# Performance work log

Hardware: AMD Instinct MI355X
Metric: run time of the kernel (lower is better)

## Reference

```python
import jax, jax.numpy as jnp
import numpy as np

N = 64          # Hilbert space dim
B = 4096        # batch of density matrices
K = 2           # number of jump operators
DT = 0.01       # time step
C = (0.0, 0.5, 1.0)
A = ((0.0, 0.0, 0.0), (0.5, 0.0, 0.0), (0.0, 1.0, 0.0))
BW = (1.0 / 6.0, 2.0 / 3.0, 1.0 / 6.0)
NEUMANN_ORDER = 2


def _dag(M):
    # real-valued reference: dagger == transpose on last two axes
    return jnp.swapaxes(M, -1, -2)


def _sandwich(M, rho):
    # M rho M^dag ; M:[N,N], rho:[B,N,N]
    return M @ rho @ _dag(M)


def _dissipator(L, rho):
    # sum_k L_k rho L_k^dag ; L:[K,N,N], rho:[B,N,N]
    return jnp.einsum('kij,bjl,kml->bim', L, rho, L)


def _neumann_ratio(Ui, Uj, I):
    # U(ci) U(cj)^{-1} with U(cj)^{-1} ~ sum_{p<=order} (I - U(cj))^p
    W = I - Uj
    inv = I
    Wp = I
    for _ in range(NEUMANN_ORDER):
        Wp = Wp @ W
        inv = inv + Wp
    return Ui @ inv


def _forward(rho0, U_half, U_one, L0, Lh, L1):
    I = jnp.eye(N, dtype=rho0.dtype)
    Umap = {0.0: I, 0.5: U_half, 1.0: U_one}
    Lmap = {0.0: L0, 0.5: Lh, 1.0: L1}

    def ratio(ci, cj):
        if ci == cj:
            return I
        if cj == 0.0:
            return Umap[ci]
        return _neumann_ratio(Umap[ci], Umap[cj], I)

    # intermediate stages rho^(i)
    stages = []
    for i, ci in enumerate(C):
        rho_i = rho0 if ci == 0.0 else _sandwich(Umap[ci], rho0)
        for j in range(i):
            a_ij = A[i][j]
            if a_ij == 0.0:
                continue
            cj = C[j]
            P_ij = ratio(ci, cj)
            rho_i = rho_i + DT * a_ij * _sandwich(P_ij, _dissipator(Lmap[cj], stages[j]))
        stages.append(rho_i)

    # output combination
    rho_new = _sandwich(Umap[1.0], rho0)
    for i, bi in enumerate(BW):
        if bi == 0.0:
            continue
        ci = C[i]
        Q_i = ratio(1.0, ci)
        rho_new = rho_new + DT * bi * _sandwich(Q_i, _dissipator(Lmap[ci], stages[i]))
    return rho_new


def setup_inputs() -> dict:
    key = jax.random.key(0)
    k1, k2, k3, k4, k5, k6 = jax.random.split(key, 6)
    I = jnp.eye(N, dtype=jnp.float32)
    rho0 = jax.random.normal(k1, (B, N, N), dtype=jnp.float32)
    rho0 = 0.5 * (rho0 + jnp.swapaxes(rho0, -1, -2))  # hermitian-like
    # no-jump propagators: near-identity so the Neumann series is sane
    U_half = I + 0.02 * jax.random.normal(k2, (N, N), dtype=jnp.float32)
    U_one = I + 0.04 * jax.random.normal(k3, (N, N), dtype=jnp.float32)
    L0 = 0.1 * jax.random.normal(k4, (K, N, N), dtype=jnp.float32)
    Lh = 0.1 * jax.random.normal(k5, (K, N, N), dtype=jnp.float32)
    L1 = 0.1 * jax.random.normal(k6, (K, N, N), dtype=jnp.float32)
    return {"rho0": rho0, "U_half": U_half, "U_one": U_one,
            "L0": L0, "Lh": Lh, "L1": L1}


def reference(rho0, U_half, U_one, L0, Lh, L1):
    return _forward(rho0, U_half, U_one, L0, Lh, L1)
```

## Files before the change

### kernel.cpp

```cpp
#include <hip/hip_runtime.h>
#include <hip/hip_bf16.h>

#define NDIM 64
#define BP   72
#define DT_  0.01f

typedef __attribute__((ext_vector_type(8)))  short bf16x8;
typedef __attribute__((ext_vector_type(16))) float f32x16;

struct Frag { bf16x8 f[4]; };


__device__ __forceinline__ unsigned short f2b(float x) {
    __hip_bfloat16 h = __float2bfloat16(x);
    return __builtin_bit_cast(unsigned short, h);
}
__device__ __forceinline__ float b2f(unsigned short u) {
    unsigned int v = (unsigned int)u << 16;
    return __builtin_bit_cast(float, v);
}
__device__ __forceinline__ unsigned int f2b2(float lo, float hi) {
    return (unsigned int)f2b(lo) | ((unsigned int)f2b(hi) << 16);
}


__device__ __forceinline__ bf16x8 ldfrag(const unsigned short* M, int rb, int j, int ln, int hq) {
    return *(const bf16x8*)&M[(rb + ln) * BP + j * 16 + hq * 8];
}

__device__ __forceinline__ void ldg_op(Frag& F, const unsigned short* __restrict__ p,
                                       int ln, int hq, int cw) {
#pragma unroll
    for (int j = 0; j < 4; ++j)
        F.f[j] = *(const bf16x8*)&p[(cw + ln) * 64 + j * 16 + hq * 8];
}

__device__ __forceinline__ void ldWfrag(Frag& F, const float* __restrict__ Uh,
                                        int ln, int hq, int cw) {
    const int n = cw + ln;
#pragma unroll
    for (int j = 0; j < 4; ++j) {
        const int k0 = j * 16 + hq * 8;
        const float* q = &Uh[n * 64 + k0];
        float4 u = *(const float4*)q;
        float4 v = *(const float4*)(q + 4);
        float wv[8] = {-u.x, -u.y, -u.z, -u.w, -v.x, -v.y, -v.z, -v.w};
#pragma unroll
        for (int e = 0; e < 8; ++e)
            if (n == k0 + e) wv[e] += 1.f;
        uint4 o;
        o.x = f2b2(wv[0], wv[1]); o.y = f2b2(wv[2], wv[3]);
        o.z = f2b2(wv[4], wv[5]); o.w = f2b2(wv[6], wv[7]);
        F.f[j] = __builtin_bit_cast(bf16x8, o);
    }
}

template <bool ACC>
__device__ __forceinline__ void ntg(const unsigned short* A, const Frag& F, f32x16& acc,
                                    int ln, int hq, int rb) {
    if (!ACC) {
#pragma unroll
        for (int r = 0; r < 16; ++r) acc[r] = 0.f;
    }
#pragma unroll
    for (int j = 0; j < 4; ++j)
        acc = __builtin_amdgcn_mfma_f32_32x32x16_bf16(ldfrag(A, rb, j, ln, hq), F.f[j], acc, 0, 0, 0);
}

__device__ __forceinline__ void ntg2(const unsigned short* A, const Frag& Fa, const Frag& Fb,
                                     f32x16& c0, f32x16& c1, int ln, int hq, int rb) {
#pragma unroll
    for (int r = 0; r < 16; ++r) { c0[r] = 0.f; c1[r] = 0.f; }
#pragma unroll
    for (int j = 0; j < 4; ++j) {
        bf16x8 a = ldfrag(A, rb, j, ln, hq);
        c0 = __builtin_amdgcn_mfma_f32_32x32x16_bf16(a, Fa.f[j], c0, 0, 0, 0);
        c1 = __builtin_amdgcn_mfma_f32_32x32x16_bf16(a, Fb.f[j], c1, 0, 0, 0);
    }
}

__device__ __forceinline__ void stT(unsigned short* D, const f32x16& v,
                                    int ln, int hq, int rw, int cw) {
#pragma unroll
    for (int g = 0; g < 4; ++g) {
        uint2 o;
        o.x = f2b2(v[4 * g + 0], v[4 * g + 1]);
        o.y = f2b2(v[4 * g + 2], v[4 * g + 3]);
        *(uint2*)&D[(cw + ln) * BP + rw + 8 * g + 4 * hq] = o;
    }
}

__device__ __forceinline__ void ldT(float* r, const unsigned short* S,
                                    int ln, int hq, int rw, int cw) {
#pragma unroll
    for (int g = 0; g < 4; ++g) {
        uint2 u = *(const uint2*)&S[(cw + ln) * BP + rw + 8 * g + 4 * hq];
        unsigned short o[4];
        *(uint2*)o = u;
#pragma unroll
        for (int j = 0; j < 4; ++j) r[4 * g + j] = b2f(o[j]);
    }
}


__global__ void __launch_bounds__(256) krk_setup(const float* __restrict__ Uh,
                                                 const float* __restrict__ U1,
                                                 const float* __restrict__ L0,
                                                 const float* __restrict__ Lh,
                                                 const float* __restrict__ L1,
                                                 unsigned short* __restrict__ ws) {
    __shared__ unsigned short sW [NDIM * BP];
    __shared__ unsigned short sWt[NDIM * BP];

    const int blk = blockIdx.x, tid = threadIdx.x;

    if (blk < 8) {
        const float* srcs[8] = {Uh, U1, L0, L0 + 4096, Lh, Lh + 4096, L1, L1 + 4096};
        const float* s = srcs[blk];
        unsigned short* d = ws + blk * 4096;
#pragma unroll
        for (int i = 0; i < 4; ++i) {
            int flat = (tid + i * 256) * 4;
            float4 v = *(const float4*)&s[flat];
            uint2 o; o.x = f2b2(v.x, v.y); o.y = f2b2(v.z, v.w);
            *(uint2*)&d[flat] = o;
        }
        return;
    }

    const int lane = tid & 63, w = tid >> 6, ln = lane & 31, hq = lane >> 5;
    const int rw = 32 * (w >> 1), cw = 32 * (w & 1);

#pragma unroll
    for (int i = 0; i < 4; ++i) {
        int flat = (tid + i * 256) * 4;
        int r = flat >> 6, c = flat & 63;
        float4 u = *(const float4*)&Uh[flat];
        float wv[4] = {-u.x, -u.y, -u.z, -u.w};
#pragma unroll
        for (int j = 0; j < 4; ++j)
            if (r == c + j) wv[j] += 1.f;
        unsigned short o[4] = {f2b(wv[0]), f2b(wv[1]), f2b(wv[2]), f2b(wv[3])};
        *(uint2*)&sW[r * BP + c] = *(uint2*)o;
#pragma unroll
        for (int j = 0; j < 4; ++j) sWt[(c + j) * BP + r] = o[j];
    }
    Frag Fw;
    ldWfrag(Fw, Uh, ln, hq, cw);
    __syncthreads();

    f32x16 t0;
    ntg<false>(sWt, Fw, t0, ln, hq, rw);
    float wts[16];
    ldT(wts, sW, ln, hq, rw, cw);
    unsigned short* ws8 = ws + 8 * 4096;
#pragma unroll
    for (int g = 0; g < 4; ++g) {
        uint2 o;
        float v0, v1;
#pragma unroll
        for (int j = 0; j < 4; j += 2) {
            int r0 = 4 * g + j, r1 = r0 + 1;
            int row0 = rw + (r0 & 3) + 8 * g + 4 * hq;
            int row1 = row0 + 1;
            v0 = ((row0 == cw + ln) ? 1.f : 0.f) + wts[r0] + t0[r0];
            v1 = ((row1 == cw + ln) ? 1.f : 0.f) + wts[r1] + t0[r1];
            if (j == 0) o.x = f2b2(v0, v1); else o.y = f2b2(v0, v1);
        }
        *(uint2*)&ws8[(cw + ln) * 64 + rw + 8 * g + 4 * hq] = o;
    }
}


__global__ void __launch_bounds__(256, 2) krk_main(const float* __restrict__ rho0,
                                                   const unsigned short* __restrict__ ws,
                                                   float* __restrict__ out) {
    __shared__ unsigned short Bb[2][4][NDIM * BP];

    const int tid = threadIdx.x;
    const int w = tid >> 6, lane = tid & 63, ln = lane & 31, hq = lane >> 5;
    const int rw = 32 * (w >> 1), cw = 32 * (w & 1);

    const float c12 = 0.5f * DT_, c16 = DT_ / 6.f, c23 = 2.f * DT_ / 3.f;

    f32x16 t0[2], t1[2], s0[2], a1[2];
    Frag Fa, Fb, Fc;

#pragma unroll
    for (int m = 0; m < 2; ++m) {
        const float* rho = rho0 + (size_t)(2 * blockIdx.x + m) * (NDIM * NDIM);
#pragma unroll
        for (int i = 0; i < 4; ++i) {
            int flat = (tid + i * 256) * 4;
            int r = flat >> 6, c = flat & 63;
            float4 v = *(const float4*)&rho[flat];
            uint2 o; o.x = f2b2(v.x, v.y); o.y = f2b2(v.z, v.w);
            *(uint2*)&Bb[m][0][r * BP + c] = o;
        }
    }
    ldg_op(Fa, ws + 2 * 4096, ln, hq, cw);
    ldg_op(Fb, ws + 3 * 4096, ln, hq, cw);
    __syncthreads();

#pragma unroll
    for (int m = 0; m < 2; ++m)
        ntg2(Bb[m][0], Fa, Fb, t0[m], t1[m], ln, hq, rw);
#pragma unroll
    for (int m = 0; m < 2; ++m) {
        stT(Bb[m][1], t0[m], ln, hq, rw, cw);
        stT(Bb[m][2], t1[m], ln, hq, rw, cw);
    }
    __syncthreads();

#pragma unroll
    for (int m = 0; m < 2; ++m) {
        ntg<false>(Bb[m][1], Fa, s0[m], ln, hq, rw);
        ntg<true >(Bb[m][2], Fb, s0[m], ln, hq, rw);
    }
#pragma unroll
    for (int m = 0; m < 2; ++m) {
        float r0s[16];
        ldT(r0s, Bb[m][0], ln, hq, rw, cw);
        f32x16 X;
#pragma unroll
        for (int r = 0; r < 16; ++r) X[r] = r0s[r] + c12 * s0[m][r];
        stT(Bb[m][0], X, ln, hq, rw, cw);
    }
    ldg_op(Fc, ws + 0 * 4096, ln, hq, cw);
    __syncthreads();

#pragma unroll
    for (int m = 0; m < 2; ++m)
        ntg<false>(Bb[m][0], Fc, t0[m], ln, hq, rw);
#pragma unroll
    for (int m = 0; m < 2; ++m)
        stT(Bb[m][3], t0[m], ln, hq, rw, cw);
    __syncthreads();

#pragma unroll
    for (int m = 0; m < 2; ++m)
        ntg<false>(Bb[m][3], Fc, t0[m], ln, hq, rw);
#pragma unroll
    for (int m = 0; m < 2; ++m)
        stT(Bb[m][1], t0[m], ln, hq, rw, cw);
    ldg_op(Fa, ws + 4 * 4096, ln, hq, cw);
    ldg_op(Fb, ws + 5 * 4096, ln, hq, cw);
    __syncthreads();

#pragma unroll
    for (int m = 0; m < 2; ++m)
        ntg2(Bb[m][1], Fa, Fb, t0[m], t1[m], ln, hq, rw);
#pragma unroll
    for (int m = 0; m < 2; ++m) {
        stT(Bb[m][2], t0[m], ln, hq, rw, cw);
        stT(Bb[m][3], t1[m], ln, hq, rw, cw);
    }
    __syncthreads();

#pragma unroll
    for (int m = 0; m < 2; ++m) {
        ntg<false>(Bb[m][2], Fa, t0[m], ln, hq, rw);
        ntg<true >(Bb[m][3], Fb, t0[m], ln, hq, rw);
    }
#pragma unroll
    for (int m = 0; m < 2; ++m)
        stT(Bb[m][1], t0[m], ln, hq, rw, cw);
    ldg_op(Fc, ws + 8 * 4096, ln, hq, cw);
    __syncthreads();

#pragma unroll
    for (int m = 0; m < 2; ++m)
        ntg<false>(Bb[m][1], Fc, t0[m], ln, hq, rw);
#pragma unroll
    for (int m = 0; m < 2; ++m)
        stT(Bb[m][2], t0[m], ln, hq, rw, cw);
    __syncthreads();

#pragma unroll
    for (int m = 0; m < 2; ++m) {
        f32x16 h1;
        ntg<false>(Bb[m][2], Fc, h1, ln, hq, rw);
        float xs[16];
        ldT(xs, Bb[m][0], ln, hq, rw, cw);
#pragma unroll
        for (int r = 0; r < 16; ++r) {
            t0[m][r] = xs[r] + (c16 - c12) * s0[m][r] + c23 * h1[r];
            t1[m][r] = xs[r] - c12 * s0[m][r] + DT_ * h1[r];
        }
        stT(Bb[m][1], t0[m], ln, hq, rw, cw);
        stT(Bb[m][3], t1[m], ln, hq, rw, cw);
    }
    ldg_op(Fc, ws + 1 * 4096, ln, hq, cw);
    __syncthreads();

#pragma unroll
    for (int m = 0; m < 2; ++m) {
        ntg<false>(Bb[m][1], Fc, t0[m], ln, hq, rw);
        ntg<false>(Bb[m][3], Fc, t1[m], ln, hq, rw);
    }
#pragma unroll
    for (int m = 0; m < 2; ++m) {
        stT(Bb[m][0], t0[m], ln, hq, rw, cw);
        stT(Bb[m][2], t1[m], ln, hq, rw, cw);
    }
    __syncthreads();

#pragma unroll
    for (int m = 0; m < 2; ++m) {
        ntg<false>(Bb[m][0], Fc, a1[m], ln, hq, rw);
        ntg<false>(Bb[m][2], Fc, t0[m], ln, hq, rw);
    }
#pragma unroll
    for (int m = 0; m < 2; ++m)
        stT(Bb[m][1], t0[m], ln, hq, rw, cw);
    ldg_op(Fa, ws + 6 * 4096, ln, hq, cw);
    ldg_op(Fb, ws + 7 * 4096, ln, hq, cw);
    __syncthreads();

#pragma unroll
    for (int m = 0; m < 2; ++m)
        ntg2(Bb[m][1], Fa, Fb, t0[m], t1[m], ln, hq, rw);
#pragma unroll
    for (int m = 0; m < 2; ++m) {
        stT(Bb[m][0], t0[m], ln, hq, rw, cw);
        stT(Bb[m][2], t1[m], ln, hq, rw, cw);
    }
    __syncthreads();

#pragma unroll
    for (int m = 0; m < 2; ++m) {
        ntg<false>(Bb[m][0], Fa, t0[m], ln, hq, rw);
        ntg<true >(Bb[m][2], Fb, t0[m], ln, hq, rw);
        float* o = out + (size_t)(2 * blockIdx.x + m) * (NDIM * NDIM);
#pragma unroll
        for (int g = 0; g < 4; ++g) {
            float4 v;
            v.x = a1[m][4 * g + 0] + c16 * t0[m][4 * g + 0];
            v.y = a1[m][4 * g + 1] + c16 * t0[m][4 * g + 1];
            v.z = a1[m][4 * g + 2] + c16 * t0[m][4 * g + 2];
            v.w = a1[m][4 * g + 3] + c16 * t0[m][4 * g + 3];
            *(float4*)&o[(cw + ln) * 64 + rw + 8 * g + 4 * hq] = v;
        }
    }
}


extern "C" void kernel_launch(void* const* d_in, const int* in_sizes, int n_in,
                              void* d_out, int out_size, void* d_ws, size_t ws_size,
                              hipStream_t stream) {
    const float* rho0 = (const float*)d_in[0];
    const float* Uh   = (const float*)d_in[1];
    const float* U1   = (const float*)d_in[2];
    const float* L0   = (const float*)d_in[3];
    const float* Lh   = (const float*)d_in[4];
    const float* L1   = (const float*)d_in[5];
    float* out = (float*)d_out;
    unsigned short* ws = (unsigned short*)d_ws;

    int Bn = in_sizes[0] / (NDIM * NDIM);

    krk_setup<<<9, 256, 0, stream>>>(Uh, U1, L0, Lh, L1, ws);
    krk_main<<<Bn / 2, 256, 0, stream>>>(rho0, ws, out);
}
```

Measured before the change: 159.1 us.

## Swizzle LDS tiles, cut buffers to three per matrix, raise occupancy

```diff
diff --git a/kernel.cpp b/kernel.cpp
--- a/kernel.cpp
+++ b/kernel.cpp
@@ -2,8 +2,9 @@
 #include <hip/hip_bf16.h>
 
 #define NDIM 64
-#define BP   72
 #define DT_  0.01f
+
+#define SWZ(row, boff) ((((row)) << 7) + ((boff) ^ (((row) & 7) << 4)))
 
 typedef __attribute__((ext_vector_type(8)))  short bf16x8;
 typedef __attribute__((ext_vector_type(16))) float f32x16;
@@ -25,7 +26,8 @@
 
 
 __device__ __forceinline__ bf16x8 ldfrag(const unsigned short* M, int rb, int j, int ln, int hq) {
-    return *(const bf16x8*)&M[(rb + ln) * BP + j * 16 + hq * 8];
+    const int row = rb + ln;
+    return *(const bf16x8*)((const char*)M + SWZ(row, 32 * j + 16 * hq));
 }
 
 __device__ __forceinline__ void ldg_op(Frag& F, const unsigned short* __restrict__ p,
@@ -81,25 +83,40 @@
 
 __device__ __forceinline__ void stT(unsigned short* D, const f32x16& v,
                                     int ln, int hq, int rw, int cw) {
+    const int row = cw + ln;
 #pragma unroll
     for (int g = 0; g < 4; ++g) {
         uint2 o;
         o.x = f2b2(v[4 * g + 0], v[4 * g + 1]);
         o.y = f2b2(v[4 * g + 2], v[4 * g + 3]);
-        *(uint2*)&D[(cw + ln) * BP + rw + 8 * g + 4 * hq] = o;
+        *(uint2*)((char*)D + SWZ(row, 2 * rw + 16 * g + 8 * hq)) = o;
     }
 }
 
 __device__ __forceinline__ void ldT(float* r, const unsigned short* S,
                                     int ln, int hq, int rw, int cw) {
+    const int row = cw + ln;
 #pragma unroll
     for (int g = 0; g < 4; ++g) {
-        uint2 u = *(const uint2*)&S[(cw + ln) * BP + rw + 8 * g + 4 * hq];
+        uint2 u = *(const uint2*)((const char*)S + SWZ(row, 2 * rw + 16 * g + 8 * hq));
         unsigned short o[4];
         *(uint2*)o = u;
 #pragma unroll
         for (int j = 0; j < 4; ++j) r[4 * g + j] = b2f(o[j]);
     }
+}
+
+__device__ __forceinline__ void ldTraw(uint2* r, const unsigned short* S,
+                                       int ln, int hq, int rw, int cw) {
+    const int row = cw + ln;
+#pragma unroll
+    for (int g = 0; g < 4; ++g)
+        r[g] = *(const uint2*)((const char*)S + SWZ(row, 2 * rw + 16 * g + 8 * hq));
+}
+__device__ __forceinline__ float rsf(const uint2* rs, int r) {
+    unsigned int wv = (r & 2) ? rs[r >> 2].y : rs[r >> 2].x;
+    unsigned short u = (r & 1) ? (unsigned short)(wv >> 16) : (unsigned short)(wv & 0xffffu);
+    return b2f(u);
 }
 
 
@@ -109,8 +126,8 @@
                                                  const float* __restrict__ Lh,
                                                  const float* __restrict__ L1,
                                                  unsigned short* __restrict__ ws) {
-    __shared__ unsigned short sW [NDIM * BP];
-    __shared__ unsigned short sWt[NDIM * BP];
+    __shared__ unsigned short sW [NDIM * NDIM];
+    __shared__ unsigned short sWt[NDIM * NDIM];
 
     const int blk = blockIdx.x, tid = threadIdx.x;
 
@@ -141,9 +158,10 @@
         for (int j = 0; j < 4; ++j)
             if (r == c + j) wv[j] += 1.f;
         unsigned short o[4] = {f2b(wv[0]), f2b(wv[1]), f2b(wv[2]), f2b(wv[3])};
-        *(uint2*)&sW[r * BP + c] = *(uint2*)o;
-#pragma unroll
-        for (int j = 0; j < 4; ++j) sWt[(c + j) * BP + r] = o[j];
+        *(uint2*)((char*)sW + SWZ(r, 2 * c)) = *(uint2*)o;
+#pragma unroll
+        for (int j = 0; j < 4; ++j)
+            *(unsigned short*)((char*)sWt + SWZ(c + j, 2 * r)) = o[j];
     }
     Frag Fw;
     ldWfrag(Fw, Uh, ln, hq, cw);
@@ -172,10 +190,10 @@
 }
 
 
-__global__ void __launch_bounds__(256, 2) krk_main(const float* __restrict__ rho0,
+__global__ void __launch_bounds__(256, 3) krk_main(const float* __restrict__ rho0,
                                                    const unsigned short* __restrict__ ws,
                                                    float* __restrict__ out) {
-    __shared__ unsigned short Bb[2][4][NDIM * BP];
+    __shared__ unsigned short Bb[2][3][NDIM * NDIM];
 
     const int tid = threadIdx.x;
     const int w = tid >> 6, lane = tid & 63, ln = lane & 31, hq = lane >> 5;
@@ -184,6 +202,7 @@
     const float c12 = 0.5f * DT_, c16 = DT_ / 6.f, c23 = 2.f * DT_ / 3.f;
 
     f32x16 t0[2], t1[2], s0[2], a1[2];
+    uint2 rs[2][4];
     Frag Fa, Fb, Fc;
 
 #pragma unroll
@@ -195,7 +214,7 @@
             int r = flat >> 6, c = flat & 63;
             float4 v = *(const float4*)&rho[flat];
             uint2 o; o.x = f2b2(v.x, v.y); o.y = f2b2(v.z, v.w);
-            *(uint2*)&Bb[m][0][r * BP + c] = o;
+            *(uint2*)((char*)Bb[m][0] + SWZ(r, 2 * c)) = o;
         }
     }
     ldg_op(Fa, ws + 2 * 4096, ln, hq, cw);
@@ -206,6 +225,9 @@
     for (int m = 0; m < 2; ++m)
         ntg2(Bb[m][0], Fa, Fb, t0[m], t1[m], ln, hq, rw);
 #pragma unroll
+    for (int m = 0; m < 2; ++m)
+        ldTraw(rs[m], Bb[m][0], ln, hq, rw, cw);
+#pragma unroll
     for (int m = 0; m < 2; ++m) {
         stT(Bb[m][1], t0[m], ln, hq, rw, cw);
         stT(Bb[m][2], t1[m], ln, hq, rw, cw);
@@ -219,11 +241,9 @@
     }
 #pragma unroll
     for (int m = 0; m < 2; ++m) {
-        float r0s[16];
-        ldT(r0s, Bb[m][0], ln, hq, rw, cw);
         f32x16 X;
 #pragma unroll
-        for (int r = 0; r < 16; ++r) X[r] = r0s[r] + c12 * s0[m][r];
+        for (int r = 0; r < 16; ++r) X[r] = rsf(rs[m], r) + c12 * s0[m][r];
         stT(Bb[m][0], X, ln, hq, rw, cw);
     }
     ldg_op(Fc, ws + 0 * 4096, ln, hq, cw);
@@ -234,103 +254,107 @@
         ntg<false>(Bb[m][0], Fc, t0[m], ln, hq, rw);
 #pragma unroll
     for (int m = 0; m < 2; ++m)
-        stT(Bb[m][3], t0[m], ln, hq, rw, cw);
-    __syncthreads();
-
-#pragma unroll
-    for (int m = 0; m < 2; ++m)
-        ntg<false>(Bb[m][3], Fc, t0[m], ln, hq, rw);
-#pragma unroll
-    for (int m = 0; m < 2; ++m)
         stT(Bb[m][1], t0[m], ln, hq, rw, cw);
+    __syncthreads();
+
+#pragma unroll
+    for (int m = 0; m < 2; ++m)
+        ntg<false>(Bb[m][1], Fc, t0[m], ln, hq, rw);
+#pragma unroll
+    for (int m = 0; m < 2; ++m)
+        stT(Bb[m][2], t0[m], ln, hq, rw, cw);
     ldg_op(Fa, ws + 4 * 4096, ln, hq, cw);
     ldg_op(Fb, ws + 5 * 4096, ln, hq, cw);
     __syncthreads();
 
 #pragma unroll
     for (int m = 0; m < 2; ++m)
-        ntg2(Bb[m][1], Fa, Fb, t0[m], t1[m], ln, hq, rw);
-#pragma unroll
-    for (int m = 0; m < 2; ++m) {
+        ntg2(Bb[m][2], Fa, Fb, t0[m], t1[m], ln, hq, rw);
+#pragma unroll
+    for (int m = 0; m < 2; ++m) {
+        stT(Bb[m][0], t0[m], ln, hq, rw, cw);
+        stT(Bb[m][1], t1[m], ln, hq, rw, cw);
+    }
+    __syncthreads();
+
+#pragma unroll
+    for (int m = 0; m < 2; ++m) {
+        ntg<false>(Bb[m][0], Fa, t0[m], ln, hq, rw);
+        ntg<true >(Bb[m][1], Fb, t0[m], ln, hq, rw);
+    }
+#pragma unroll
+    for (int m = 0; m < 2; ++m)
         stT(Bb[m][2], t0[m], ln, hq, rw, cw);
-        stT(Bb[m][3], t1[m], ln, hq, rw, cw);
-    }
-    __syncthreads();
-
-#pragma unroll
-    for (int m = 0; m < 2; ++m) {
-        ntg<false>(Bb[m][2], Fa, t0[m], ln, hq, rw);
-        ntg<true >(Bb[m][3], Fb, t0[m], ln, hq, rw);
-    }
-#pragma unroll
-    for (int m = 0; m < 2; ++m)
-        stT(Bb[m][1], t0[m], ln, hq, rw, cw);
     ldg_op(Fc, ws + 8 * 4096, ln, hq, cw);
     __syncthreads();
 
 #pragma unroll
     for (int m = 0; m < 2; ++m)
+        ntg<false>(Bb[m][2], Fc, t0[m], ln, hq, rw);
+#pragma unroll
+    for (int m = 0; m < 2; ++m)
+        stT(Bb[m][0], t0[m], ln, hq, rw, cw);
+    __syncthreads();
+
+#pragma unroll
+    for (int m = 0; m < 2; ++m) {
+        f32x16 h1;
+        ntg<false>(Bb[m][0], Fc, h1, ln, hq, rw);
+        f32x16 M1, M2;
+#pragma unroll
+        for (int r = 0; r < 16; ++r) {
+            float rv = rsf(rs[m], r);
+            M1[r] = rv + c16 * s0[m][r] + c23 * h1[r];
+            M2[r] = rv + DT_ * h1[r];
+        }
+        stT(Bb[m][1], M1, ln, hq, rw, cw);
+        stT(Bb[m][2], M2, ln, hq, rw, cw);
+    }
+    ldg_op(Fc, ws + 1 * 4096, ln, hq, cw);
+    __syncthreads();
+
+#pragma unroll
+    for (int m = 0; m < 2; ++m)
         ntg<false>(Bb[m][1], Fc, t0[m], ln, hq, rw);
 #pragma unroll
     for (int m = 0; m < 2; ++m)
+        stT(Bb[m][0], t0[m], ln, hq, rw, cw);
+    __syncthreads();
+
+#pragma unroll
+    for (int m = 0; m < 2; ++m) {
+        ntg<false>(Bb[m][0], Fc, a1[m], ln, hq, rw);
+        ntg<false>(Bb[m][2], Fc, t1[m], ln, hq, rw);
+    }
+#pragma unroll
+    for (int m = 0; m < 2; ++m)
+        stT(Bb[m][1], t1[m], ln, hq, rw, cw);
+    __syncthreads();
+
+#pragma unroll
+    for (int m = 0; m < 2; ++m)
+        ntg<false>(Bb[m][1], Fc, t0[m], ln, hq, rw);
+#pragma unroll
+    for (int m = 0; m < 2; ++m)
         stT(Bb[m][2], t0[m], ln, hq, rw, cw);
-    __syncthreads();
-
-#pragma unroll
-    for (int m = 0; m < 2; ++m) {
-        f32x16 h1;
-        ntg<false>(Bb[m][2], Fc, h1, ln, hq, rw);
-        float xs[16];
-        ldT(xs, Bb[m][0], ln, hq, rw, cw);
-#pragma unroll
-        for (int r = 0; r < 16; ++r) {
-            t0[m][r] = xs[r] + (c16 - c12) * s0[m][r] + c23 * h1[r];
-            t1[m][r] = xs[r] - c12 * s0[m][r] + DT_ * h1[r];
-        }
-        stT(Bb[m][1], t0[m], ln, hq, rw, cw);
-        stT(Bb[m][3], t1[m], ln, hq, rw, cw);
-    }
-    ldg_op(Fc, ws + 1 * 4096, ln, hq, cw);
-    __syncthreads();
-
-#pragma unroll
-    for (int m = 0; m < 2; ++m) {
-        ntg<false>(Bb[m][1], Fc, t0[m], ln, hq, rw);
-        ntg<false>(Bb[m][3], Fc, t1[m], ln, hq, rw);
-    }
-#pragma unroll
-    for (int m = 0; m < 2; ++m) {
-        stT(Bb[m][0], t0[m], ln, hq, rw, cw);
-        stT(Bb[m][2], t1[m], ln, hq, rw, cw);
-    }
-    __syncthreads();
-
-#pragma unroll
-    for (int m = 0; m < 2; ++m) {
-        ntg<false>(Bb[m][0], Fc, a1[m], ln, hq, rw);
-        ntg<false>(Bb[m][2], Fc, t0[m], ln, hq, rw);
-    }
-#pragma unroll
-    for (int m = 0; m < 2; ++m)
-        stT(Bb[m][1], t0[m], ln, hq, rw, cw);
     ldg_op(Fa, ws + 6 * 4096, ln, hq, cw);
     ldg_op(Fb, ws + 7 * 4096, ln, hq, cw);
     __syncthreads();
 
 #pragma unroll
     for (int m = 0; m < 2; ++m)
-        ntg2(Bb[m][1], Fa, Fb, t0[m], t1[m], ln, hq, rw);
+        ntg2(Bb[m][2], Fa, Fb, t0[m], t1[m], ln, hq, rw);
 #pragma unroll
     for (int m = 0; m < 2; ++m) {
         stT(Bb[m][0], t0[m], ln, hq, rw, cw);
-        stT(Bb[m][2], t1[m], ln, hq, rw, cw);
+        stT(Bb[m][1], t1[m], ln, hq, rw, cw);
     }
     __syncthreads();
 
 #pragma unroll
     for (int m = 0; m < 2; ++m) {
         ntg<false>(Bb[m][0], Fa, t0[m], ln, hq, rw);
-        ntg<true >(Bb[m][2], Fb, t0[m], ln, hq, rw);
+        ntg<true >(Bb[m][1], Fb, t0[m], ln, hq, rw);
         float* o = out + (size_t)(2 * blockIdx.x + m) * (NDIM * NDIM);
 #pragma unroll
         for (int g = 0; g < 4; ++g) {
```

Measured after the change: 177.2 us. +11.4%, slower.

## Collapse RK stages into sum of precomputed sandwich operators per batch

Applied to the files above, without the earlier changes.

```diff
diff --git a/kernel.cpp b/kernel.cpp
--- a/kernel.cpp
+++ b/kernel.cpp
@@ -4,6 +4,7 @@
 #define NDIM 64
 #define BP   72
 #define DT_  0.01f
+#define NTERM 23
 
 typedef __attribute__((ext_vector_type(8)))  short bf16x8;
 typedef __attribute__((ext_vector_type(16))) float f32x16;
@@ -33,6 +34,27 @@
 #pragma unroll
     for (int j = 0; j < 4; ++j)
         F.f[j] = *(const bf16x8*)&p[(cw + ln) * 64 + j * 16 + hq * 8];
+}
+
+__device__ __forceinline__ void ldsF(Frag& F, const unsigned short* p, int ln, int hq, int cw) {
+#pragma unroll
+    for (int j = 0; j < 4; ++j)
+        F.f[j] = *(const bf16x8*)&p[(cw + ln) * BP + j * 16 + hq * 8];
+}
+
+__device__ __forceinline__ void ldg_opF32(Frag& F, const float* __restrict__ P,
+                                          int ln, int hq, int cw) {
+    const int n = cw + ln;
+#pragma unroll
+    for (int j = 0; j < 4; ++j) {
+        const float* q = &P[n * 64 + j * 16 + hq * 8];
+        float4 u = *(const float4*)q;
+        float4 v = *(const float4*)(q + 4);
+        uint4 o;
+        o.x = f2b2(u.x, u.y); o.y = f2b2(u.z, u.w);
+        o.z = f2b2(v.x, v.y); o.w = f2b2(v.z, v.w);
+        F.f[j] = __builtin_bit_cast(bf16x8, o);
+    }
 }
 
 __device__ __forceinline__ void ldWfrag(Frag& F, const float* __restrict__ Uh,
@@ -67,16 +89,12 @@
         acc = __builtin_amdgcn_mfma_f32_32x32x16_bf16(ldfrag(A, rb, j, ln, hq), F.f[j], acc, 0, 0, 0);
 }
 
-__device__ __forceinline__ void ntg2(const unsigned short* A, const Frag& Fa, const Frag& Fb,
-                                     f32x16& c0, f32x16& c1, int ln, int hq, int rb) {
-#pragma unroll
-    for (int r = 0; r < 16; ++r) { c0[r] = 0.f; c1[r] = 0.f; }
-#pragma unroll
-    for (int j = 0; j < 4; ++j) {
-        bf16x8 a = ldfrag(A, rb, j, ln, hq);
-        c0 = __builtin_amdgcn_mfma_f32_32x32x16_bf16(a, Fa.f[j], c0, 0, 0, 0);
-        c1 = __builtin_amdgcn_mfma_f32_32x32x16_bf16(a, Fb.f[j], c1, 0, 0, 0);
-    }
+__device__ __forceinline__ f32x16 ntg_reg(const Frag& A, const Frag& F, const f32x16& Z) {
+    f32x16 a = __builtin_amdgcn_mfma_f32_32x32x16_bf16(A.f[0], F.f[0], Z, 0, 0, 0);
+#pragma unroll
+    for (int j = 1; j < 4; ++j)
+        a = __builtin_amdgcn_mfma_f32_32x32x16_bf16(A.f[j], F.f[j], a, 0, 0, 0);
+    return a;
 }
 
 __device__ __forceinline__ void stT(unsigned short* D, const f32x16& v,
@@ -90,6 +108,15 @@
     }
 }
 
+__device__ __forceinline__ void stN(unsigned short* D, const f32x16& v,
+                                    int ln, int hq, int rw, int cw) {
+#pragma unroll
+    for (int r = 0; r < 16; ++r) {
+        int row = rw + (r & 3) + 8 * (r >> 2) + 4 * hq;
+        D[row * BP + (cw + ln)] = f2b(v[r]);
+    }
+}
+
 __device__ __forceinline__ void ldT(float* r, const unsigned short* S,
                                     int ln, int hq, int rw, int cw) {
 #pragma unroll
@@ -99,6 +126,17 @@
         *(uint2*)o = u;
 #pragma unroll
         for (int j = 0; j < 4; ++j) r[4 * g + j] = b2f(o[j]);
+    }
+}
+
+__device__ __forceinline__ void emit(unsigned short* __restrict__ g, const f32x16& v, float s,
+                                     int ln, int hq, int rw, int cw) {
+#pragma unroll
+    for (int gq = 0; gq < 4; ++gq) {
+        uint2 o;
+        o.x = f2b2(s * v[4 * gq + 0], s * v[4 * gq + 1]);
+        o.y = f2b2(s * v[4 * gq + 2], s * v[4 * gq + 3]);
+        *(uint2*)&g[(cw + ln) * 64 + rw + 8 * gq + 4 * hq] = o;
     }
 }
 
@@ -109,236 +147,207 @@
                                                  const float* __restrict__ Lh,
                                                  const float* __restrict__ L1,
                                                  unsigned short* __restrict__ ws) {
-    __shared__ unsigned short sW [NDIM * BP];
-    __shared__ unsigned short sWt[NDIM * BP];
-
-    const int blk = blockIdx.x, tid = threadIdx.x;
-
-    if (blk < 8) {
-        const float* srcs[8] = {Uh, U1, L0, L0 + 4096, Lh, Lh + 4096, L1, L1 + 4096};
-        const float* s = srcs[blk];
-        unsigned short* d = ws + blk * 4096;
-#pragma unroll
-        for (int i = 0; i < 4; ++i) {
-            int flat = (tid + i * 256) * 4;
-            float4 v = *(const float4*)&s[flat];
-            uint2 o; o.x = f2b2(v.x, v.y); o.y = f2b2(v.z, v.w);
-            *(uint2*)&d[flat] = o;
-        }
-        return;
-    }
-
+    __shared__ unsigned short B[7][NDIM * BP];
+
+    const int tid = threadIdx.x;
     const int lane = tid & 63, w = tid >> 6, ln = lane & 31, hq = lane >> 5;
     const int rw = 32 * (w >> 1), cw = 32 * (w & 1);
+
+    const float c12 = 0.5f * DT_, c16 = DT_ / 6.f, c23 = 2.f * DT_ / 3.f;
+    const float sA = sqrtf(c16);
+    const float sB = sqrtf(c23);
+    const float sC = sqrtf(c23 * c12);
+    const float sD = sqrtf(c16 * DT_);
+    const float sE = sqrtf(c16 * DT_ * c12);
 
 #pragma unroll
     for (int i = 0; i < 4; ++i) {
         int flat = (tid + i * 256) * 4;
         int r = flat >> 6, c = flat & 63;
         float4 u = *(const float4*)&Uh[flat];
-        float wv[4] = {-u.x, -u.y, -u.z, -u.w};
-#pragma unroll
-        for (int j = 0; j < 4; ++j)
-            if (r == c + j) wv[j] += 1.f;
-        unsigned short o[4] = {f2b(wv[0]), f2b(wv[1]), f2b(wv[2]), f2b(wv[3])};
-        *(uint2*)&sW[r * BP + c] = *(uint2*)o;
-#pragma unroll
-        for (int j = 0; j < 4; ++j) sWt[(c + j) * BP + r] = o[j];
-    }
-    Frag Fw;
+        const float* uf = (const float*)&u;
+        float wv[4];
+#pragma unroll
+        for (int j = 0; j < 4; ++j) wv[j] = ((r == c + j) ? 1.f : 0.f) - uf[j];
+#pragma unroll
+        for (int j = 0; j < 4; ++j) B[0][(c + j) * BP + r] = f2b(uf[j]);
+        uint2 ow; ow.x = f2b2(wv[0], wv[1]); ow.y = f2b2(wv[2], wv[3]);
+        *(uint2*)&B[4][r * BP + c] = ow;
+#pragma unroll
+        for (int j = 0; j < 4; ++j) B[5][(c + j) * BP + r] = f2b(wv[j]);
+
+        float4 p = *(const float4*)&U1[flat];
+        const float* pf = (const float*)&p;
+#pragma unroll
+        for (int j = 0; j < 4; ++j) B[1][(c + j) * BP + r] = f2b(pf[j]);
+        uint2 oq; oq.x = f2b2(p.x, p.y); oq.y = f2b2(p.z, p.w);
+        *(uint2*)&ws[flat] = oq;
+
+        float4 a = *(const float4*)&L0[flat];
+        const float* af = (const float*)&a;
+#pragma unroll
+        for (int j = 0; j < 4; ++j) B[2][(c + j) * BP + r] = f2b(af[j]);
+        float4 b = *(const float4*)&L0[4096 + flat];
+        const float* bf = (const float*)&b;
+#pragma unroll
+        for (int j = 0; j < 4; ++j) B[3][(c + j) * BP + r] = f2b(bf[j]);
+    }
+
+    Frag FUh, FU1, FLh0, FLh1, F10, F11, Fw;
+    ldg_opF32(FUh,  Uh,        ln, hq, cw);
+    ldg_opF32(FU1,  U1,        ln, hq, cw);
+    ldg_opF32(FLh0, Lh,        ln, hq, cw);
+    ldg_opF32(FLh1, Lh + 4096, ln, hq, cw);
+    ldg_opF32(F10,  L1,        ln, hq, cw);
+    ldg_opF32(F11,  L1 + 4096, ln, hq, cw);
     ldWfrag(Fw, Uh, ln, hq, cw);
     __syncthreads();
 
-    f32x16 t0;
-    ntg<false>(sWt, Fw, t0, ln, hq, rw);
-    float wts[16];
-    ldT(wts, sW, ln, hq, rw, cw);
-    unsigned short* ws8 = ws + 8 * 4096;
-#pragma unroll
-    for (int g = 0; g < 4; ++g) {
-        uint2 o;
-        float v0, v1;
-#pragma unroll
-        for (int j = 0; j < 4; j += 2) {
-            int r0 = 4 * g + j, r1 = r0 + 1;
-            int row0 = rw + (r0 & 3) + 8 * g + 4 * hq;
-            int row1 = row0 + 1;
-            v0 = ((row0 == cw + ln) ? 1.f : 0.f) + wts[r0] + t0[r0];
-            v1 = ((row1 == cw + ln) ? 1.f : 0.f) + wts[r1] + t0[r1];
-            if (j == 0) o.x = f2b2(v0, v1); else o.y = f2b2(v0, v1);
-        }
-        *(uint2*)&ws8[(cw + ln) * 64 + rw + 8 * g + 4 * hq] = o;
-    }
-}
-
-
-__global__ void __launch_bounds__(256, 2) krk_main(const float* __restrict__ rho0,
+    f32x16 e;
+
+    {
+        f32x16 t0;
+        ntg<false>(B[5], Fw, t0, ln, hq, rw);
+        float wts[16];
+        ldT(wts, B[4], ln, hq, rw, cw);
+#pragma unroll
+        for (int g = 0; g < 4; ++g) {
+            float vv[4];
+#pragma unroll
+            for (int i = 0; i < 4; ++i) {
+                int r = 4 * g + i;
+                int row = rw + i + 8 * g + 4 * hq;
+                vv[i] = ((row == cw + ln) ? 1.f : 0.f) + wts[r] + t0[r];
+            }
+            uint2 o; o.x = f2b2(vv[0], vv[1]); o.y = f2b2(vv[2], vv[3]);
+            *(uint2*)&B[6][(cw + ln) * BP + rw + 8 * g + 4 * hq] = o;
+        }
+    }
+    ntg<false>(B[2], FU1, e, ln, hq, rw); emit(ws + 1 * 4096, e, sA, ln, hq, rw, cw);
+    ntg<false>(B[3], FU1, e, ln, hq, rw); emit(ws + 2 * 4096, e, sA, ln, hq, rw, cw);
+    ntg<false>(B[1], F10, e, ln, hq, rw); emit(ws + 9 * 4096, e, sA, ln, hq, rw, cw);
+    ntg<false>(B[1], F11, e, ln, hq, rw); emit(ws + 10 * 4096, e, sA, ln, hq, rw, cw);
+    __syncthreads();
+
+    Frag FV; ldsF(FV, B[6], ln, hq, cw);
+
+    ntg<false>(B[2], FUh, e, ln, hq, rw); stN(B[4], e, ln, hq, rw, cw);
+    ntg<false>(B[3], FUh, e, ln, hq, rw); stN(B[5], e, ln, hq, rw, cw);
+    __syncthreads();
+
+    ntg<false>(B[0], FLh0, e, ln, hq, rw); stN(B[1], e, ln, hq, rw, cw);
+    ntg<false>(B[0], FLh1, e, ln, hq, rw); stN(B[2], e, ln, hq, rw, cw);
+    __syncthreads();
+
+    ntg<false>(B[1], FV, e, ln, hq, rw); stN(B[3], e, ln, hq, rw, cw);
+    ntg<false>(B[2], FV, e, ln, hq, rw); stN(B[0], e, ln, hq, rw, cw);
+    __syncthreads();
+
+    ntg<false>(B[3], FU1, e, ln, hq, rw); emit(ws + 3 * 4096, e, sB, ln, hq, rw, cw); stN(B[1], e, ln, hq, rw, cw);
+    ntg<false>(B[0], FU1, e, ln, hq, rw); emit(ws + 4 * 4096, e, sB, ln, hq, rw, cw); stN(B[2], e, ln, hq, rw, cw);
+    __syncthreads();
+
+    ntg<false>(B[1], F10, e, ln, hq, rw); emit(ws + 11 * 4096, e, sD, ln, hq, rw, cw);
+    ntg<false>(B[2], F10, e, ln, hq, rw); emit(ws + 12 * 4096, e, sD, ln, hq, rw, cw);
+    ntg<false>(B[1], F11, e, ln, hq, rw); emit(ws + 13 * 4096, e, sD, ln, hq, rw, cw);
+    ntg<false>(B[2], F11, e, ln, hq, rw); emit(ws + 14 * 4096, e, sD, ln, hq, rw, cw);
+    ntg<false>(B[4], FLh0, e, ln, hq, rw); stN(B[0], e, ln, hq, rw, cw);
+    ntg<false>(B[5], FLh0, e, ln, hq, rw); stN(B[3], e, ln, hq, rw, cw);
+    __syncthreads();
+
+    ntg<false>(B[0], FV, e, ln, hq, rw); stN(B[1], e, ln, hq, rw, cw);
+    ntg<false>(B[3], FV, e, ln, hq, rw); stN(B[2], e, ln, hq, rw, cw);
+    __syncthreads();
+
+    ntg<false>(B[1], FU1, e, ln, hq, rw); emit(ws + 5 * 4096, e, sC, ln, hq, rw, cw); stN(B[0], e, ln, hq, rw, cw);
+    ntg<false>(B[2], FU1, e, ln, hq, rw); emit(ws + 6 * 4096, e, sC, ln, hq, rw, cw); stN(B[3], e, ln, hq, rw, cw);
+    __syncthreads();
+
+    ntg<false>(B[0], F10, e, ln, hq, rw); emit(ws + 15 * 4096, e, sE, ln, hq, rw, cw);
+    ntg<false>(B[3], F10, e, ln, hq, rw); emit(ws + 16 * 4096, e, sE, ln, hq, rw, cw);
+    ntg<false>(B[0], F11, e, ln, hq, rw); emit(ws + 19 * 4096, e, sE, ln, hq, rw, cw);
+    ntg<false>(B[3], F11, e, ln, hq, rw); emit(ws + 20 * 4096, e, sE, ln, hq, rw, cw);
+    ntg<false>(B[4], FLh1, e, ln, hq, rw); stN(B[1], e, ln, hq, rw, cw);
+    ntg<false>(B[5], FLh1, e, ln, hq, rw); stN(B[2], e, ln, hq, rw, cw);
+    __syncthreads();
+
+    ntg<false>(B[1], FV, e, ln, hq, rw); stN(B[4], e, ln, hq, rw, cw);
+    ntg<false>(B[2], FV, e, ln, hq, rw); stN(B[5], e, ln, hq, rw, cw);
+    __syncthreads();
+
+    ntg<false>(B[4], FU1, e, ln, hq, rw); emit(ws + 7 * 4096, e, sC, ln, hq, rw, cw); stN(B[1], e, ln, hq, rw, cw);
+    ntg<false>(B[5], FU1, e, ln, hq, rw); emit(ws + 8 * 4096, e, sC, ln, hq, rw, cw); stN(B[2], e, ln, hq, rw, cw);
+    __syncthreads();
+
+    ntg<false>(B[1], F10, e, ln, hq, rw); emit(ws + 17 * 4096, e, sE, ln, hq, rw, cw);
+    ntg<false>(B[2], F10, e, ln, hq, rw); emit(ws + 18 * 4096, e, sE, ln, hq, rw, cw);
+    ntg<false>(B[1], F11, e, ln, hq, rw); emit(ws + 21 * 4096, e, sE, ln, hq, rw, cw);
+    ntg<false>(B[2], F11, e, ln, hq, rw); emit(ws + 22 * 4096, e, sE, ln, hq, rw, cw);
+}
+
+
+__global__ void __launch_bounds__(256, 3) krk_main(const float* __restrict__ rho0,
                                                    const unsigned short* __restrict__ ws,
                                                    float* __restrict__ out) {
-    __shared__ unsigned short Bb[2][4][NDIM * BP];
+    __shared__ unsigned short S[2][2][NDIM * BP];
 
     const int tid = threadIdx.x;
     const int w = tid >> 6, lane = tid & 63, ln = lane & 31, hq = lane >> 5;
     const int rw = 32 * (w >> 1), cw = 32 * (w & 1);
 
-    const float c12 = 0.5f * DT_, c16 = DT_ / 6.f, c23 = 2.f * DT_ / 3.f;
-
-    f32x16 t0[2], t1[2], s0[2], a1[2];
-    Frag Fa, Fb, Fc;
-
+    Frag Ar[2];
 #pragma unroll
     for (int m = 0; m < 2; ++m) {
-        const float* rho = rho0 + (size_t)(2 * blockIdx.x + m) * (NDIM * NDIM);
-#pragma unroll
-        for (int i = 0; i < 4; ++i) {
-            int flat = (tid + i * 256) * 4;
-            int r = flat >> 6, c = flat & 63;
-            float4 v = *(const float4*)&rho[flat];
-            uint2 o; o.x = f2b2(v.x, v.y); o.y = f2b2(v.z, v.w);
-            *(uint2*)&Bb[m][0][r * BP + c] = o;
-        }
-    }
-    ldg_op(Fa, ws + 2 * 4096, ln, hq, cw);
-    ldg_op(Fb, ws + 3 * 4096, ln, hq, cw);
-    __syncthreads();
-
-#pragma unroll
-    for (int m = 0; m < 2; ++m)
-        ntg2(Bb[m][0], Fa, Fb, t0[m], t1[m], ln, hq, rw);
+        const float* rho = rho0 + (size_t)(2 * blockIdx.x + m) * 4096;
+        const float* q0 = &rho[(rw + ln) * 64];
+#pragma unroll
+        for (int j = 0; j < 4; ++j) {
+            const float* q = q0 + j * 16 + hq * 8;
+            float4 u = *(const float4*)q;
+            float4 v = *(const float4*)(q + 4);
+            uint4 o;
+            o.x = f2b2(u.x, u.y); o.y = f2b2(u.z, u.w);
+            o.z = f2b2(v.x, v.y); o.w = f2b2(v.z, v.w);
+            Ar[m].f[j] = __builtin_bit_cast(bf16x8, o);
+        }
+    }
+
+    f32x16 Z;
+#pragma unroll
+    for (int r = 0; r < 16; ++r) Z[r] = 0.f;
+    f32x16 acc[2] = {Z, Z};
+
+    Frag F[3];
+    ldg_op(F[0], ws, ln, hq, cw);
+
+#pragma unroll
+    for (int t = 0; t < NTERM; ++t) {
+        if (t > 0) {
+#pragma unroll
+            for (int m = 0; m < 2; ++m)
+                ntg<true>(S[m][(t - 1) & 1], F[(t - 1) % 3], acc[m], ln, hq, rw);
+        }
+#pragma unroll
+        for (int m = 0; m < 2; ++m) {
+            f32x16 tv = ntg_reg(Ar[m], F[t % 3], Z);
+            stT(S[m][t & 1], tv, ln, hq, rw, cw);
+        }
+        if (t + 1 < NTERM)
+            ldg_op(F[(t + 1) % 3], ws + (size_t)(t + 1) * 4096, ln, hq, cw);
+        __syncthreads();
+    }
+
 #pragma unroll
     for (int m = 0; m < 2; ++m) {
-        stT(Bb[m][1], t0[m], ln, hq, rw, cw);
-        stT(Bb[m][2], t1[m], ln, hq, rw, cw);
-    }
-    __syncthreads();
-
-#pragma unroll
-    for (int m = 0; m < 2; ++m) {
-        ntg<false>(Bb[m][1], Fa, s0[m], ln, hq, rw);
-        ntg<true >(Bb[m][2], Fb, s0[m], ln, hq, rw);
-    }
-#pragma unroll
-    for (int m = 0; m < 2; ++m) {
-        float r0s[16];
-        ldT(r0s, Bb[m][0], ln, hq, rw, cw);
-        f32x16 X;
-#pragma unroll
-        for (int r = 0; r < 16; ++r) X[r] = r0s[r] + c12 * s0[m][r];
-        stT(Bb[m][0], X, ln, hq, rw, cw);
-    }
-    ldg_op(Fc, ws + 0 * 4096, ln, hq, cw);
-    __syncthreads();
-
-#pragma unroll
-    for (int m = 0; m < 2; ++m)
-        ntg<false>(Bb[m][0], Fc, t0[m], ln, hq, rw);
-#pragma unroll
-    for (int m = 0; m < 2; ++m)
-        stT(Bb[m][3], t0[m], ln, hq, rw, cw);
-    __syncthreads();
-
-#pragma unroll
-    for (int m = 0; m < 2; ++m)
-        ntg<false>(Bb[m][3], Fc, t0[m], ln, hq, rw);
-#pragma unroll
-    for (int m = 0; m < 2; ++m)
-        stT(Bb[m][1], t0[m], ln, hq, rw, cw);
-    ldg_op(Fa, ws + 4 * 4096, ln, hq, cw);
-    ldg_op(Fb, ws + 5 * 4096, ln, hq, cw);
-    __syncthreads();
-
-#pragma unroll
-    for (int m = 0; m < 2; ++m)
-        ntg2(Bb[m][1], Fa, Fb, t0[m], t1[m], ln, hq, rw);
-#pragma unroll
-    for (int m = 0; m < 2; ++m) {
-        stT(Bb[m][2], t0[m], ln, hq, rw, cw);
-        stT(Bb[m][3], t1[m], ln, hq, rw, cw);
-    }
-    __syncthreads();
-
-#pragma unroll
-    for (int m = 0; m < 2; ++m) {
-        ntg<false>(Bb[m][2], Fa, t0[m], ln, hq, rw);
-        ntg<true >(Bb[m][3], Fb, t0[m], ln, hq, rw);
-    }
-#pragma unroll
-    for (int m = 0; m < 2; ++m)
-        stT(Bb[m][1], t0[m], ln, hq, rw, cw);
-    ldg_op(Fc, ws + 8 * 4096, ln, hq, cw);
-    __syncthreads();
-
-#pragma unroll
-    for (int m = 0; m < 2; ++m)
-        ntg<false>(Bb[m][1], Fc, t0[m], ln, hq, rw);
-#pragma unroll
-    for (int m = 0; m < 2; ++m)
-        stT(Bb[m][2], t0[m], ln, hq, rw, cw);
-    __syncthreads();
-
-#pragma unroll
-    for (int m = 0; m < 2; ++m) {
-        f32x16 h1;
-        ntg<false>(Bb[m][2], Fc, h1, ln, hq, rw);
-        float xs[16];
-        ldT(xs, Bb[m][0], ln, hq, rw, cw);
-#pragma unroll
-        for (int r = 0; r < 16; ++r) {
-            t0[m][r] = xs[r] + (c16 - c12) * s0[m][r] + c23 * h1[r];
-            t1[m][r] = xs[r] - c12 * s0[m][r] + DT_ * h1[r];
-        }
-        stT(Bb[m][1], t0[m], ln, hq, rw, cw);
-        stT(Bb[m][3], t1[m], ln, hq, rw, cw);
-    }
-    ldg_op(Fc, ws + 1 * 4096, ln, hq, cw);
-    __syncthreads();
-
-#pragma unroll
-    for (int m = 0; m < 2; ++m) {
-        ntg<false>(Bb[m][1], Fc, t0[m], ln, hq, rw);
-        ntg<false>(Bb[m][3], Fc, t1[m], ln, hq, rw);
-    }
-#pragma unroll
-    for (int m = 0; m < 2; ++m) {
-        stT(Bb[m][0], t0[m], ln, hq, rw, cw);
-        stT(Bb[m][2], t1[m], ln, hq, rw, cw);
-    }
-    __syncthreads();
-
-#pragma unroll
-    for (int m = 0; m < 2; ++m) {
-        ntg<false>(Bb[m][0], Fc, a1[m], ln, hq, rw);
-        ntg<false>(Bb[m][2], Fc, t0[m], ln, hq, rw);
-    }
-#pragma unroll
-    for (int m = 0; m < 2; ++m)
-        stT(Bb[m][1], t0[m], ln, hq, rw, cw);
-    ldg_op(Fa, ws + 6 * 4096, ln, hq, cw);
-    ldg_op(Fb, ws + 7 * 4096, ln, hq, cw);
-    __syncthreads();
-
-#pragma unroll
-    for (int m = 0; m < 2; ++m)
-        ntg2(Bb[m][1], Fa, Fb, t0[m], t1[m], ln, hq, rw);
-#pragma unroll
-    for (int m = 0; m < 2; ++m) {
-        stT(Bb[m][0], t0[m], ln, hq, rw, cw);
-        stT(Bb[m][2], t1[m], ln, hq, rw, cw);
-    }
-    __syncthreads();
-
-#pragma unroll
-    for (int m = 0; m < 2; ++m) {
-        ntg<false>(Bb[m][0], Fa, t0[m], ln, hq, rw);
-        ntg<true >(Bb[m][2], Fb, t0[m], ln, hq, rw);
-        float* o = out + (size_t)(2 * blockIdx.x + m) * (NDIM * NDIM);
+        ntg<true>(S[m][(NTERM - 1) & 1], F[(NTERM - 1) % 3], acc[m], ln, hq, rw);
+        float* o = out + (size_t)(2 * blockIdx.x + m) * 4096;
 #pragma unroll
         for (int g = 0; g < 4; ++g) {
             float4 v;
-            v.x = a1[m][4 * g + 0] + c16 * t0[m][4 * g + 0];
-            v.y = a1[m][4 * g + 1] + c16 * t0[m][4 * g + 1];
-            v.z = a1[m][4 * g + 2] + c16 * t0[m][4 * g + 2];
-            v.w = a1[m][4 * g + 3] + c16 * t0[m][4 * g + 3];
+            v.x = acc[m][4 * g + 0];
+            v.y = acc[m][4 * g + 1];
+            v.z = acc[m][4 * g + 2];
+            v.w = acc[m][4 * g + 3];
             *(float4*)&o[(cw + ln) * 64 + rw + 8 * g + 4 * hq] = v;
         }
     }
@@ -359,6 +368,6 @@
 
     int Bn = in_sizes[0] / (NDIM * NDIM);
 
-    krk_setup<<<9, 256, 0, stream>>>(Uh, U1, L0, Lh, L1, ws);
+    krk_setup<<<1, 256, 0, stream>>>(Uh, U1, L0, Lh, L1, ws);
     krk_main<<<Bn / 2, 256, 0, stream>>>(rho0, ws, out);
 }
```

Result: slower. 236.4 us (+48.6%).
